# Performance work log

Hardware: AMD Instinct MI355X
Metric: run time of the kernel (lower is better)

Reference implementation:

```python
import jax, jax.numpy as jnp
import numpy as np

NUM_HEADS = 8
TOP_K = 32
LN_EPS = 1e-5
RENORM_EPS = 1e-5


def _split_heads(x):
    # [B, S, D] -> [B, H, S, d]
    B, S, D = x.shape
    return x.reshape(B, S, NUM_HEADS, D // NUM_HEADS).transpose(0, 2, 1, 3)


def setup_inputs() -> dict:
    key = jax.random.key(0)
    k1, k2, k3, k4 = jax.random.split(key, 4)
    B, S, D, H = 2, 2048, 1024, NUM_HEADS
    q = jax.random.normal(k1, (B, S, D), dtype=jnp.float32)
    k = jax.random.normal(k2, (B, S, D), dtype=jnp.float32)
    v = jax.random.normal(k3, (B, S, D), dtype=jnp.float32)
    attention_weight = jax.random.normal(k4, (B, H, S, S), dtype=jnp.float32)
    gamma = jnp.ones((D,), dtype=jnp.float32)
    beta = jnp.zeros((D,), dtype=jnp.float32)
    return {"q": q, "k": k, "v": v, "attention_weight": attention_weight,
            "gamma": gamma, "beta": beta}


def reference(q, k, v, attention_weight, gamma, beta):
    B, S, D = q.shape
    qh = _split_heads(q)  # [B,H,S,d]
    kh = _split_heads(k)
    vh = _split_heads(v)
    # Unscaled QK^T (faithful to source: no /sqrt(d))
    scores = jnp.einsum("bhqd,bhkd->bhqk", qh, kh)
    probs = jax.nn.softmax(scores, axis=-1)
    # top-k mask via double argsort: rank of each key by descending weight
    rank = jnp.argsort(jnp.argsort(-attention_weight, axis=-1), axis=-1)
    top_mask = (rank < TOP_K).astype(probs.dtype)
    probs = probs * top_mask
    probs = probs / (jnp.sum(probs, axis=-1, keepdims=True) + RENORM_EPS)
    out = jnp.einsum("bhqk,bhkd->bhqd", probs, vh)
    out = out.transpose(0, 2, 1, 3).reshape(B, S, D)
    # LayerNorm over last dim
    mu = jnp.mean(out, axis=-1, keepdims=True)
    var = jnp.var(out, axis=-1, keepdims=True)
    out = (out - mu) * jax.lax.rsqrt(var + LN_EPS) * gamma + beta
    return out
```

## Files before the change

### kernel.cpp

```cpp
#include <hip/hip_runtime.h>
#include <stdint.h>

#define BB 2
#define SS 2048
#define DD 1024
#define HH 8
#define HD 128
#define TOPK 32
#define ROWS (BB*HH*SS)
#define BH 16

typedef float f32x4 __attribute__((ext_vector_type(4)));
typedef _Float16 f16x8 __attribute__((ext_vector_type(8)));
typedef _Float16 f16x4 __attribute__((ext_vector_type(4)));

__device__ __forceinline__ void gload_lds16(const _Float16* g, _Float16* l) {
    __builtin_amdgcn_global_load_lds(
        (const __attribute__((address_space(1))) void*)g,
        (__attribute__((address_space(3))) void*)l, 16, 0, 0);
}

__global__ __launch_bounds__(256) void cvt_kernel(const float* __restrict__ q,
                                                  const float* __restrict__ k,
                                                  const float* __restrict__ v,
                                                  _Float16* __restrict__ q16,
                                                  _Float16* __restrict__ k16,
                                                  _Float16* __restrict__ v16) {
    const int row = blockIdx.x;
    const int b = row >> 11, s = row & 2047;
    const int t = threadIdx.x;
    const int h = t >> 5, d4 = (t & 31) * 4;
    const size_t src = (size_t)row * DD + t * 4;
    const size_t dst = ((size_t)(b * HH + h) * SS + s) * HD + d4;
    float4 f;
    f = *(const float4*)(q + src);
    *(f16x4*)(q16 + dst) = (f16x4){(_Float16)f.x,(_Float16)f.y,(_Float16)f.z,(_Float16)f.w};
    f = *(const float4*)(k + src);
    *(f16x4*)(k16 + dst) = (f16x4){(_Float16)f.x,(_Float16)f.y,(_Float16)f.z,(_Float16)f.w};
    f = *(const float4*)(v + src);
    *(f16x4*)(v16 + dst) = (f16x4){(_Float16)f.x,(_Float16)f.y,(_Float16)f.z,(_Float16)f.w};
}

__global__ __launch_bounds__(256) void topk_kernel(const float* __restrict__ aw,
                                                   int* __restrict__ idx_out) {
    const int row = blockIdx.x;
    const float* p = aw + (size_t)row * SS;
    const int t = threadIdx.x;
    float4 v0 = *(const float4*)(p + 4 * t);
    float4 v1 = *(const float4*)(p + 1024 + 4 * t);
    float vals[8] = {v0.x, v0.y, v0.z, v0.w, v1.x, v1.y, v1.z, v1.w};
    unsigned long long key[8];
#pragma unroll
    for (int i = 0; i < 8; i++) {
        int e = (i < 4) ? (4 * t + i) : (1024 + 4 * t + (i - 4));
        unsigned u = __float_as_uint(vals[i]);
        unsigned sk = (u & 0x80000000u) ? ~u : (u | 0x80000000u);
        key[i] = ((unsigned long long)sk << 11) | (unsigned)(2047 - e);
    }
    __shared__ int s_cnt;
    __shared__ int s_red[4];
    __shared__ unsigned long long s_cand[256];
    const int lane = t & 63, wv = t >> 6;

    unsigned thr0 = __float_as_uint(1.76f) | 0x80000000u;
    unsigned long long T = ((unsigned long long)thr0 << 11) | 2047ull;

    if (t == 0) s_cnt = 0;
    __syncthreads();
#pragma unroll
    for (int i = 0; i < 8; i++) {
        if (key[i] > T) {
            int pos = atomicAdd(&s_cnt, 1);
            if (pos < 256) s_cand[pos] = key[i];
        }
    }
    __syncthreads();

    if (s_cnt < TOPK || s_cnt > 256) {
        unsigned long long lo = 0, hi = ~0ull;
        if (s_cnt > 256) lo = T; else hi = T;
        T = lo + ((hi - lo) >> 1);
        for (int it = 0; it < 40; ++it) {
            int c = 0;
#pragma unroll
            for (int i = 0; i < 8; i++) c += (key[i] > T) ? 1 : 0;
            for (int off = 32; off; off >>= 1) c += __shfl_down(c, off, 64);
            if (lane == 0) s_red[wv] = c;
            __syncthreads();
            int tot = s_red[0] + s_red[1] + s_red[2] + s_red[3];
            if (tot >= TOPK && tot <= 256) break;
            if (tot > 256) lo = T; else hi = T;
            T = lo + ((hi - lo) >> 1);
            __syncthreads();
        }
        if (t == 0) s_cnt = 0;
        __syncthreads();
#pragma unroll
        for (int i = 0; i < 8; i++) {
            if (key[i] > T) {
                int pos = atomicAdd(&s_cnt, 1);
                if (pos < 256) s_cand[pos] = key[i];
            }
        }
        __syncthreads();
    }

    const int C = s_cnt < 256 ? s_cnt : 256;
    if (t < C) {
        unsigned long long mk = s_cand[t];
        int rank = 0;
        for (int j = 0; j < C; ++j)
            rank += (s_cand[j] > mk) ? 1 : 0;
        if (rank < TOPK)
            idx_out[(size_t)row * TOPK + rank] = 2047 - (int)(mk & 2047ull);
    }
}

__global__ __launch_bounds__(256) void stats_kernel(const _Float16* __restrict__ q16,
                                                    const _Float16* __restrict__ k16,
                                                    float* __restrict__ ws_m,
                                                    float* __restrict__ ws_l) {
    __shared__ __align__(16) _Float16 Ks[2][64 * 128];
    const int xcd = blockIdx.x & 7;
    const int r = blockIdx.x >> 3;
    const int bh = xcd * 2 + (r & 1);
    const int rr = r >> 1;
    const int qt = rr & 15;
    const int quarter = rr >> 4;
    const int t = threadIdx.x;
    const int wv = t >> 6, lane = t & 63;
    const int l16 = lane & 15, quad = lane >> 4;

    const _Float16* qb = q16 + ((size_t)bh * SS + qt * 128 + wv * 32 + l16) * HD;
    f16x8 af[2][4];
#pragma unroll
    for (int a = 0; a < 2; a++)
#pragma unroll
        for (int ks = 0; ks < 4; ks++)
            af[a][ks] = *(const f16x8*)(qb + a * 16 * HD + ks * 32 + quad * 8);

    const int lr = lane >> 4, lc = lane & 15;
    int srco[4];
#pragma unroll
    for (int i = 0; i < 4; i++) {
        int x = ((i & 1) * 4) + lr;
        srco[i] = (wv * 16 + i * 4 + lr) * HD + ((lc ^ x) * 8);
    }
    const _Float16* kb = k16 + (size_t)bh * SS * HD;

    int rdoff[4];
#pragma unroll
    for (int ks = 0; ks < 4; ks++)
        rdoff[ks] = (((ks * 4 + quad) ^ (l16 & 7)) * 8);

    float mrun[2][4], lrun[2][4];
#pragma unroll
    for (int a = 0; a < 2; a++)
#pragma unroll
        for (int r2 = 0; r2 < 4; r2++) { mrun[a][r2] = -INFINITY; lrun[a][r2] = 0.f; }

    {
        const _Float16* src = kb + (size_t)(quarter * 8) * 64 * HD;
#pragma unroll
        for (int i = 0; i < 4; i++)
            gload_lds16(src + srco[i], &Ks[0][(wv * 4 + i) * 512]);
    }
    __syncthreads();

    int cur = 0;
    for (int tt = 0; tt < 8; ++tt) {
        if (tt < 7) {
            const _Float16* src = kb + (size_t)(quarter * 8 + tt + 1) * 64 * HD;
#pragma unroll
            for (int i = 0; i < 4; i++)
                gload_lds16(src + srco[i], &Ks[cur ^ 1][(wv * 4 + i) * 512]);
        }
        f32x4 acc[2][4];
#pragma unroll
        for (int a = 0; a < 2; a++)
#pragma unroll
            for (int n = 0; n < 4; n++) acc[a][n] = (f32x4){0.f, 0.f, 0.f, 0.f};
#pragma unroll
        for (int ks = 0; ks < 4; ++ks) {
            f16x8 bfr[4];
#pragma unroll
            for (int n = 0; n < 4; n++)
                bfr[n] = *(const f16x8*)&Ks[cur][(n * 16 + l16) * HD + rdoff[ks]];
#pragma unroll
            for (int a = 0; a < 2; a++)
#pragma unroll
                for (int n = 0; n < 4; n++)
                    acc[a][n] = __builtin_amdgcn_mfma_f32_16x16x32_f16(af[a][ks], bfr[n], acc[a][n], 0, 0, 0);
        }
#pragma unroll
        for (int a = 0; a < 2; a++) {
#pragma unroll
            for (int r2 = 0; r2 < 4; r2++) {
                float tm = fmaxf(fmaxf(acc[a][0][r2], acc[a][1][r2]),
                                 fmaxf(acc[a][2][r2], acc[a][3][r2]));
#pragma unroll
                for (int off = 1; off < 16; off <<= 1) tm = fmaxf(tm, __shfl_xor(tm, off, 64));
                float tl = 0.f;
#pragma unroll
                for (int n = 0; n < 4; n++) tl += __expf(acc[a][n][r2] - tm);
#pragma unroll
                for (int off = 1; off < 16; off <<= 1) tl += __shfl_xor(tl, off, 64);
                float mo = mrun[a][r2];
                float mn = fmaxf(mo, tm);
                lrun[a][r2] = lrun[a][r2] * __expf(mo - mn) + tl * __expf(tm - mn);
                mrun[a][r2] = mn;
            }
        }
        __syncthreads();
        cur ^= 1;
    }

    if (l16 == 0) {
#pragma unroll
        for (int a = 0; a < 2; a++)
#pragma unroll
            for (int r2 = 0; r2 < 4; r2++) {
                int rrow = qt * 128 + wv * 32 + a * 16 + quad * 4 + r2;
                size_t g = (size_t)quarter * ROWS + (size_t)bh * SS + rrow;
                ws_m[g] = mrun[a][r2];
                ws_l[g] = lrun[a][r2];
            }
    }
}

__global__ __launch_bounds__(128) void attnout_kernel(const float* __restrict__ q,
                                                      const float* __restrict__ k,
                                                      const _Float16* __restrict__ v16,
                                                      const int* __restrict__ idx_ws,
                                                      const float* __restrict__ ws_m,
                                                      const float* __restrict__ ws_l,
                                                      float* __restrict__ out) {
    const int bh = blockIdx.x & 15;
    const int s = blockIdx.x >> 4;
    const int R = (bh << 11) | s;
    const int b = bh >> 3, h = bh & 7;
    const int t = threadIdx.x;
    __shared__ float q_l[128];
    __shared__ int idx_l[32];
    __shared__ float e_l[32];
    __shared__ float w_l[32];
    __shared__ __align__(16) float s_pv[4][128];
    const float* qrow = q + ((size_t)(b * SS + s) * DD + h * HD);
    q_l[t] = qrow[t];
    if (t < 32) idx_l[t] = idx_ws[(size_t)R * TOPK + t];
    __syncthreads();
    float m = ws_m[R];
    m = fmaxf(m, ws_m[(size_t)ROWS + R]);
    m = fmaxf(m, ws_m[2 * (size_t)ROWS + R]);
    m = fmaxf(m, ws_m[3 * (size_t)ROWS + R]);
    float Z = 0.f;
#pragma unroll
    for (int qr = 0; qr < 4; ++qr)
        Z += ws_l[(size_t)qr * ROWS + R] * __expf(ws_m[(size_t)qr * ROWS + R] - m);

    const int l32 = t & 31, g = t >> 5;
    float4 q4 = *(const float4*)&q_l[l32 * 4];
    const float* kb = k + ((size_t)b * SS * DD + h * HD);
#pragma unroll
    for (int p = 0; p < 8; ++p) {
        int i = p * 4 + g;
        int ki = idx_l[i];
        float4 kv = *(const float4*)(kb + (size_t)ki * DD + l32 * 4);
        float d = q4.x * kv.x + q4.y * kv.y + q4.z * kv.z + q4.w * kv.w;
#pragma unroll
        for (int off = 1; off < 32; off <<= 1) d += __shfl_xor(d, off, 64);
        if (l32 == 0) e_l[i] = __expf(d - m);
    }
    __syncthreads();
    if (t < 32) {
        float e = e_l[t];
        float ssum = e;
#pragma unroll
        for (int off = 1; off < 32; off <<= 1) ssum += __shfl_xor(ssum, off, 64);
        float den = ssum + 1e-5f * Z;
        w_l[t] = e / den;
    }
    __syncthreads();
    const _Float16* vb = v16 + (size_t)bh * SS * HD;
    float a0 = 0.f, a1 = 0.f, a2 = 0.f, a3 = 0.f;
#pragma unroll
    for (int p = 0; p < 8; ++p) {
        int i = p * 4 + g;
        f16x4 hv = *(const f16x4*)(vb + (size_t)idx_l[i] * HD + l32 * 4);
        float w = w_l[i];
        a0 += w * (float)hv[0];
        a1 += w * (float)hv[1];
        a2 += w * (float)hv[2];
        a3 += w * (float)hv[3];
    }
    *(float4*)&s_pv[g][l32 * 4] = make_float4(a0, a1, a2, a3);
    __syncthreads();
    out[((size_t)(b * SS + s) * DD) + h * HD + t] =
        s_pv[0][t] + s_pv[1][t] + s_pv[2][t] + s_pv[3][t];
}

__global__ __launch_bounds__(256) void ln_kernel(float* __restrict__ out,
                                                 const float* __restrict__ gamma,
                                                 const float* __restrict__ beta) {
    const int row = blockIdx.x;
    float* p = out + (size_t)row * DD;
    const int t = threadIdx.x;
    float x[4];
#pragma unroll
    for (int i = 0; i < 4; i++) x[i] = p[t + 256 * i];
    float sum = x[0] + x[1] + x[2] + x[3];
    __shared__ float red[4];
    const int lane = t & 63, wv = t >> 6;
    for (int off = 32; off; off >>= 1) sum += __shfl_down(sum, off, 64);
    if (lane == 0) red[wv] = sum;
    __syncthreads();
    float mean = (red[0] + red[1] + red[2] + red[3]) * (1.f / DD);
    __syncthreads();
    float vs = 0.f;
#pragma unroll
    for (int i = 0; i < 4; i++) { float d = x[i] - mean; vs += d * d; }
    for (int off = 32; off; off >>= 1) vs += __shfl_down(vs, off, 64);
    if (lane == 0) red[wv] = vs;
    __syncthreads();
    float var = (red[0] + red[1] + red[2] + red[3]) * (1.f / DD);
    float inv = rsqrtf(var + 1e-5f);
#pragma unroll
    for (int i = 0; i < 4; i++) {
        int c = t + 256 * i;
        p[c] = (x[i] - mean) * inv * gamma[c] + beta[c];
    }
}

extern "C" void kernel_launch(void* const* d_in, const int* in_sizes, int n_in,
                              void* d_out, int out_size, void* d_ws, size_t ws_size,
                              hipStream_t stream) {
    const float* q = (const float*)d_in[0];
    const float* k = (const float*)d_in[1];
    const float* v = (const float*)d_in[2];
    const float* aw = (const float*)d_in[3];
    const float* gamma = (const float*)d_in[4];
    const float* beta = (const float*)d_in[5];
    float* out = (float*)d_out;

    int* idx_ws = (int*)d_ws;
    float* ws_m = (float*)((char*)d_ws + ((size_t)4 << 20));
    float* ws_l = ws_m + (size_t)4 * ROWS;
    _Float16* q16 = (_Float16*)((char*)d_ws + ((size_t)8 << 20));
    _Float16* k16 = q16 + (size_t)BH * SS * HD;
    _Float16* v16 = k16 + (size_t)BH * SS * HD;

    hipLaunchKernelGGL(cvt_kernel, dim3(BB * SS), dim3(256), 0, stream, q, k, v, q16, k16, v16);
    hipLaunchKernelGGL(topk_kernel, dim3(ROWS), dim3(256), 0, stream, aw, idx_ws);
    hipLaunchKernelGGL(stats_kernel, dim3(1024), dim3(256), 0, stream, q16, k16, ws_m, ws_l);
    hipLaunchKernelGGL(attnout_kernel, dim3(ROWS), dim3(128), 0, stream, q, k, v16, idx_ws, ws_m, ws_l, out);
    hipLaunchKernelGGL(ln_kernel, dim3(BB * SS), dim3(256), 0, stream, out, gamma, beta);
}
```

Baseline: 525.0 us.

## Fuse cvt, topk and stats kernels into one launch with in-kernel fp32 K/Q conversion

Merges the conversion, top-k selection and softmax-stats kernels into a single launch, splitting the work by block index. The stats path now reads fp32 Q and K directly and converts to fp16 in registers before writing K into swizzled LDS, so the separate Q/K fp16 copies are dropped. The aim is to cut kernel launch gaps and the Q/K conversion write-and-reread traffic, and to let top-k blocks overlap with the stats blocks. In exchange, the stats blocks each read twice as many bytes of K and repeat the conversion, and register-staged prefetch replaces the async global-to-LDS loads.

```diff
diff --git a/kernel.cpp b/kernel.cpp
--- a/kernel.cpp
+++ b/kernel.cpp
@@ -10,221 +10,239 @@
 #define ROWS (BB*HH*SS)
 #define BH 16
 
+#define NSTATS 1024
+#define NCVT   4096
+#define NTOPK  32768
+
 typedef float f32x4 __attribute__((ext_vector_type(4)));
 typedef _Float16 f16x8 __attribute__((ext_vector_type(8)));
 typedef _Float16 f16x4 __attribute__((ext_vector_type(4)));
 
-__device__ __forceinline__ void gload_lds16(const _Float16* g, _Float16* l) {
-    __builtin_amdgcn_global_load_lds(
-        (const __attribute__((address_space(1))) void*)g,
-        (__attribute__((address_space(3))) void*)l, 16, 0, 0);
-}
-
-__global__ __launch_bounds__(256) void cvt_kernel(const float* __restrict__ q,
-                                                  const float* __restrict__ k,
-                                                  const float* __restrict__ v,
-                                                  _Float16* __restrict__ q16,
-                                                  _Float16* __restrict__ k16,
-                                                  _Float16* __restrict__ v16) {
-    const int row = blockIdx.x;
-    const int b = row >> 11, s = row & 2047;
-    const int t = threadIdx.x;
-    const int h = t >> 5, d4 = (t & 31) * 4;
-    const size_t src = (size_t)row * DD + t * 4;
-    const size_t dst = ((size_t)(b * HH + h) * SS + s) * HD + d4;
-    float4 f;
-    f = *(const float4*)(q + src);
-    *(f16x4*)(q16 + dst) = (f16x4){(_Float16)f.x,(_Float16)f.y,(_Float16)f.z,(_Float16)f.w};
-    f = *(const float4*)(k + src);
-    *(f16x4*)(k16 + dst) = (f16x4){(_Float16)f.x,(_Float16)f.y,(_Float16)f.z,(_Float16)f.w};
-    f = *(const float4*)(v + src);
-    *(f16x4*)(v16 + dst) = (f16x4){(_Float16)f.x,(_Float16)f.y,(_Float16)f.z,(_Float16)f.w};
-}
-
-__global__ __launch_bounds__(256) void topk_kernel(const float* __restrict__ aw,
-                                                   int* __restrict__ idx_out) {
-    const int row = blockIdx.x;
-    const float* p = aw + (size_t)row * SS;
-    const int t = threadIdx.x;
-    float4 v0 = *(const float4*)(p + 4 * t);
-    float4 v1 = *(const float4*)(p + 1024 + 4 * t);
-    float vals[8] = {v0.x, v0.y, v0.z, v0.w, v1.x, v1.y, v1.z, v1.w};
-    unsigned long long key[8];
-#pragma unroll
-    for (int i = 0; i < 8; i++) {
-        int e = (i < 4) ? (4 * t + i) : (1024 + 4 * t + (i - 4));
-        unsigned u = __float_as_uint(vals[i]);
-        unsigned sk = (u & 0x80000000u) ? ~u : (u | 0x80000000u);
-        key[i] = ((unsigned long long)sk << 11) | (unsigned)(2047 - e);
-    }
-    __shared__ int s_cnt;
-    __shared__ int s_red[4];
-    __shared__ unsigned long long s_cand[256];
-    const int lane = t & 63, wv = t >> 6;
-
-    unsigned thr0 = __float_as_uint(1.76f) | 0x80000000u;
-    unsigned long long T = ((unsigned long long)thr0 << 11) | 2047ull;
-
-    if (t == 0) s_cnt = 0;
-    __syncthreads();
-#pragma unroll
-    for (int i = 0; i < 8; i++) {
-        if (key[i] > T) {
-            int pos = atomicAdd(&s_cnt, 1);
-            if (pos < 256) s_cand[pos] = key[i];
-        }
-    }
-    __syncthreads();
-
-    if (s_cnt < TOPK || s_cnt > 256) {
-        unsigned long long lo = 0, hi = ~0ull;
-        if (s_cnt > 256) lo = T; else hi = T;
-        T = lo + ((hi - lo) >> 1);
-        for (int it = 0; it < 40; ++it) {
-            int c = 0;
-#pragma unroll
-            for (int i = 0; i < 8; i++) c += (key[i] > T) ? 1 : 0;
-            for (int off = 32; off; off >>= 1) c += __shfl_down(c, off, 64);
-            if (lane == 0) s_red[wv] = c;
-            __syncthreads();
-            int tot = s_red[0] + s_red[1] + s_red[2] + s_red[3];
-            if (tot >= TOPK && tot <= 256) break;
-            if (tot > 256) lo = T; else hi = T;
-            T = lo + ((hi - lo) >> 1);
-            __syncthreads();
-        }
-        if (t == 0) s_cnt = 0;
-        __syncthreads();
-#pragma unroll
-        for (int i = 0; i < 8; i++) {
-            if (key[i] > T) {
-                int pos = atomicAdd(&s_cnt, 1);
-                if (pos < 256) s_cand[pos] = key[i];
-            }
-        }
-        __syncthreads();
-    }
-
-    const int C = s_cnt < 256 ? s_cnt : 256;
-    if (t < C) {
-        unsigned long long mk = s_cand[t];
-        int rank = 0;
-        for (int j = 0; j < C; ++j)
-            rank += (s_cand[j] > mk) ? 1 : 0;
-        if (rank < TOPK)
-            idx_out[(size_t)row * TOPK + rank] = 2047 - (int)(mk & 2047ull);
-    }
-}
-
-__global__ __launch_bounds__(256) void stats_kernel(const _Float16* __restrict__ q16,
-                                                    const _Float16* __restrict__ k16,
+__global__ __launch_bounds__(256) void fused_kernel(const float* __restrict__ q,
+                                                    const float* __restrict__ k,
+                                                    const float* __restrict__ v,
+                                                    const float* __restrict__ aw,
+                                                    _Float16* __restrict__ v16,
+                                                    int* __restrict__ idx_out,
                                                     float* __restrict__ ws_m,
                                                     float* __restrict__ ws_l) {
     __shared__ __align__(16) _Float16 Ks[2][64 * 128];
-    const int xcd = blockIdx.x & 7;
-    const int r = blockIdx.x >> 3;
-    const int bh = xcd * 2 + (r & 1);
-    const int rr = r >> 1;
-    const int qt = rr & 15;
-    const int quarter = rr >> 4;
+    const int bid = blockIdx.x;
     const int t = threadIdx.x;
-    const int wv = t >> 6, lane = t & 63;
-    const int l16 = lane & 15, quad = lane >> 4;
-
-    const _Float16* qb = q16 + ((size_t)bh * SS + qt * 128 + wv * 32 + l16) * HD;
-    f16x8 af[2][4];
-#pragma unroll
-    for (int a = 0; a < 2; a++)
+
+    if (bid < NSTATS) {
+        const int xcd = bid & 7;
+        const int r = bid >> 3;
+        const int bh = xcd * 2 + (r & 1);
+        const int rr = r >> 1;
+        const int qt = rr & 15;
+        const int quarter = rr >> 4;
+        const int b = bh >> 3, h = bh & 7;
+        const int wv = t >> 6, lane = t & 63;
+        const int l16 = lane & 15, quad = lane >> 4;
+
+        f16x8 af[2][4];
+#pragma unroll
+        for (int a = 0; a < 2; a++)
+#pragma unroll
+            for (int ks = 0; ks < 4; ks++) {
+                const float* qs = q + (size_t)(b * SS + qt * 128 + wv * 32 + a * 16 + l16) * DD
+                                    + h * HD + ks * 32 + quad * 8;
+                float4 f0 = *(const float4*)qs;
+                float4 f1 = *(const float4*)(qs + 4);
+                af[a][ks] = (f16x8){(_Float16)f0.x,(_Float16)f0.y,(_Float16)f0.z,(_Float16)f0.w,
+                                    (_Float16)f1.x,(_Float16)f1.y,(_Float16)f1.z,(_Float16)f1.w};
+            }
+
+        const int srow = t >> 2, cgrp = t & 3;
+        const float* kb = k + (size_t)b * SS * DD + h * HD;
+
+        int rdoff[4];
 #pragma unroll
         for (int ks = 0; ks < 4; ks++)
-            af[a][ks] = *(const f16x8*)(qb + a * 16 * HD + ks * 32 + quad * 8);
-
-    const int lr = lane >> 4, lc = lane & 15;
-    int srco[4];
-#pragma unroll
-    for (int i = 0; i < 4; i++) {
-        int x = ((i & 1) * 4) + lr;
-        srco[i] = (wv * 16 + i * 4 + lr) * HD + ((lc ^ x) * 8);
-    }
-    const _Float16* kb = k16 + (size_t)bh * SS * HD;
-
-    int rdoff[4];
-#pragma unroll
-    for (int ks = 0; ks < 4; ks++)
-        rdoff[ks] = (((ks * 4 + quad) ^ (l16 & 7)) * 8);
-
-    float mrun[2][4], lrun[2][4];
-#pragma unroll
-    for (int a = 0; a < 2; a++)
-#pragma unroll
-        for (int r2 = 0; r2 < 4; r2++) { mrun[a][r2] = -INFINITY; lrun[a][r2] = 0.f; }
+            rdoff[ks] = (((ks * 4 + quad) ^ (l16 & 7)) * 8);
+
+        float mrun[2][4], lrun[2][4];
+#pragma unroll
+        for (int a = 0; a < 2; a++)
+#pragma unroll
+            for (int r2 = 0; r2 < 4; r2++) { mrun[a][r2] = -INFINITY; lrun[a][r2] = 0.f; }
+
+        {
+            const float* src = kb + (size_t)(quarter * 8 * 64 + srow) * DD;
+            float4 fr[8];
+#pragma unroll
+            for (int c = 0; c < 4; c++) {
+                int cc = cgrp * 4 + c;
+                fr[c * 2]     = *(const float4*)(src + cc * 8);
+                fr[c * 2 + 1] = *(const float4*)(src + cc * 8 + 4);
+            }
+#pragma unroll
+            for (int c = 0; c < 4; c++) {
+                int cc = cgrp * 4 + c;
+                f16x8 w = {(_Float16)fr[c*2].x,(_Float16)fr[c*2].y,(_Float16)fr[c*2].z,(_Float16)fr[c*2].w,
+                           (_Float16)fr[c*2+1].x,(_Float16)fr[c*2+1].y,(_Float16)fr[c*2+1].z,(_Float16)fr[c*2+1].w};
+                *(f16x8*)&Ks[0][srow * 128 + ((cc ^ (srow & 7)) * 8)] = w;
+            }
+        }
+        __syncthreads();
+
+        int cur = 0;
+        for (int tt = 0; tt < 8; ++tt) {
+            float4 nf[8];
+            if (tt < 7) {
+                const float* src = kb + (size_t)((quarter * 8 + tt + 1) * 64 + srow) * DD;
+#pragma unroll
+                for (int c = 0; c < 4; c++) {
+                    int cc = cgrp * 4 + c;
+                    nf[c * 2]     = *(const float4*)(src + cc * 8);
+                    nf[c * 2 + 1] = *(const float4*)(src + cc * 8 + 4);
+                }
+            }
+            f32x4 acc[2][4];
+#pragma unroll
+            for (int a = 0; a < 2; a++)
+#pragma unroll
+                for (int n = 0; n < 4; n++) acc[a][n] = (f32x4){0.f, 0.f, 0.f, 0.f};
+#pragma unroll
+            for (int ks = 0; ks < 4; ++ks) {
+                f16x8 bfr[4];
+#pragma unroll
+                for (int n = 0; n < 4; n++)
+                    bfr[n] = *(const f16x8*)&Ks[cur][(n * 16 + l16) * 128 + rdoff[ks]];
+#pragma unroll
+                for (int a = 0; a < 2; a++)
+#pragma unroll
+                    for (int n = 0; n < 4; n++)
+                        acc[a][n] = __builtin_amdgcn_mfma_f32_16x16x32_f16(af[a][ks], bfr[n], acc[a][n], 0, 0, 0);
+            }
+#pragma unroll
+            for (int a = 0; a < 2; a++) {
+#pragma unroll
+                for (int r2 = 0; r2 < 4; r2++) {
+                    float tm = fmaxf(fmaxf(acc[a][0][r2], acc[a][1][r2]),
+                                     fmaxf(acc[a][2][r2], acc[a][3][r2]));
+#pragma unroll
+                    for (int off = 1; off < 16; off <<= 1) tm = fmaxf(tm, __shfl_xor(tm, off, 64));
+                    float tl = 0.f;
+#pragma unroll
+                    for (int n = 0; n < 4; n++) tl += __expf(acc[a][n][r2] - tm);
+#pragma unroll
+                    for (int off = 1; off < 16; off <<= 1) tl += __shfl_xor(tl, off, 64);
+                    float mo = mrun[a][r2];
+                    float mn = fmaxf(mo, tm);
+                    lrun[a][r2] = lrun[a][r2] * __expf(mo - mn) + tl * __expf(tm - mn);
+                    mrun[a][r2] = mn;
+                }
+            }
+            if (tt < 7) {
+#pragma unroll
+                for (int c = 0; c < 4; c++) {
+                    int cc = cgrp * 4 + c;
+                    f16x8 w = {(_Float16)nf[c*2].x,(_Float16)nf[c*2].y,(_Float16)nf[c*2].z,(_Float16)nf[c*2].w,
+                               (_Float16)nf[c*2+1].x,(_Float16)nf[c*2+1].y,(_Float16)nf[c*2+1].z,(_Float16)nf[c*2+1].w};
+                    *(f16x8*)&Ks[cur ^ 1][srow * 128 + ((cc ^ (srow & 7)) * 8)] = w;
+                }
+            }
+            __syncthreads();
+            cur ^= 1;
+        }
+
+        if (l16 == 0) {
+#pragma unroll
+            for (int a = 0; a < 2; a++)
+#pragma unroll
+                for (int r2 = 0; r2 < 4; r2++) {
+                    int rrow = qt * 128 + wv * 32 + a * 16 + quad * 4 + r2;
+                    size_t g = (size_t)quarter * ROWS + (size_t)bh * SS + rrow;
+                    ws_m[g] = mrun[a][r2];
+                    ws_l[g] = lrun[a][r2];
+                }
+        }
+        return;
+    }
+
+    if (bid < NSTATS + NCVT) {
+        const int row = bid - NSTATS;
+        const int b = row >> 11, s = row & 2047;
+        const int h = t >> 5, d4 = (t & 31) * 4;
+        float4 f = *(const float4*)(v + (size_t)row * DD + t * 4);
+        *(f16x4*)(v16 + ((size_t)(b * HH + h) * SS + s) * HD + d4) =
+            (f16x4){(_Float16)f.x,(_Float16)f.y,(_Float16)f.z,(_Float16)f.w};
+        return;
+    }
 
     {
-        const _Float16* src = kb + (size_t)(quarter * 8) * 64 * HD;
-#pragma unroll
-        for (int i = 0; i < 4; i++)
-            gload_lds16(src + srco[i], &Ks[0][(wv * 4 + i) * 512]);
-    }
-    __syncthreads();
-
-    int cur = 0;
-    for (int tt = 0; tt < 8; ++tt) {
-        if (tt < 7) {
-            const _Float16* src = kb + (size_t)(quarter * 8 + tt + 1) * 64 * HD;
-#pragma unroll
-            for (int i = 0; i < 4; i++)
-                gload_lds16(src + srco[i], &Ks[cur ^ 1][(wv * 4 + i) * 512]);
-        }
-        f32x4 acc[2][4];
-#pragma unroll
-        for (int a = 0; a < 2; a++)
-#pragma unroll
-            for (int n = 0; n < 4; n++) acc[a][n] = (f32x4){0.f, 0.f, 0.f, 0.f};
-#pragma unroll
-        for (int ks = 0; ks < 4; ++ks) {
-            f16x8 bfr[4];
-#pragma unroll
-            for (int n = 0; n < 4; n++)
-                bfr[n] = *(const f16x8*)&Ks[cur][(n * 16 + l16) * HD + rdoff[ks]];
-#pragma unroll
-            for (int a = 0; a < 2; a++)
-#pragma unroll
-                for (int n = 0; n < 4; n++)
-                    acc[a][n] = __builtin_amdgcn_mfma_f32_16x16x32_f16(af[a][ks], bfr[n], acc[a][n], 0, 0, 0);
-        }
-#pragma unroll
-        for (int a = 0; a < 2; a++) {
-#pragma unroll
-            for (int r2 = 0; r2 < 4; r2++) {
-                float tm = fmaxf(fmaxf(acc[a][0][r2], acc[a][1][r2]),
-                                 fmaxf(acc[a][2][r2], acc[a][3][r2]));
-#pragma unroll
-                for (int off = 1; off < 16; off <<= 1) tm = fmaxf(tm, __shfl_xor(tm, off, 64));
-                float tl = 0.f;
-#pragma unroll
-                for (int n = 0; n < 4; n++) tl += __expf(acc[a][n][r2] - tm);
-#pragma unroll
-                for (int off = 1; off < 16; off <<= 1) tl += __shfl_xor(tl, off, 64);
-                float mo = mrun[a][r2];
-                float mn = fmaxf(mo, tm);
-                lrun[a][r2] = lrun[a][r2] * __expf(mo - mn) + tl * __expf(tm - mn);
-                mrun[a][r2] = mn;
-            }
-        }
+        const int row = bid - (NSTATS + NCVT);
+        const float* p = aw + (size_t)row * SS;
+        int* s_cnt = (int*)&Ks[0][0];
+        int* s_red = (int*)&Ks[0][8];
+        unsigned long long* s_cand = (unsigned long long*)&Ks[0][32];
+        float4 v0 = *(const float4*)(p + 4 * t);
+        float4 v1 = *(const float4*)(p + 1024 + 4 * t);
+        float vals[8] = {v0.x, v0.y, v0.z, v0.w, v1.x, v1.y, v1.z, v1.w};
+        unsigned long long key[8];
+#pragma unroll
+        for (int i = 0; i < 8; i++) {
+            int e = (i < 4) ? (4 * t + i) : (1024 + 4 * t + (i - 4));
+            unsigned u = __float_as_uint(vals[i]);
+            unsigned sk = (u & 0x80000000u) ? ~u : (u | 0x80000000u);
+            key[i] = ((unsigned long long)sk << 11) | (unsigned)(2047 - e);
+        }
+        const int lane = t & 63, wv = t >> 6;
+
+        unsigned thr0 = __float_as_uint(1.76f) | 0x80000000u;
+        unsigned long long T = ((unsigned long long)thr0 << 11) | 2047ull;
+
+        if (t == 0) *s_cnt = 0;
         __syncthreads();
-        cur ^= 1;
-    }
-
-    if (l16 == 0) {
-#pragma unroll
-        for (int a = 0; a < 2; a++)
-#pragma unroll
-            for (int r2 = 0; r2 < 4; r2++) {
-                int rrow = qt * 128 + wv * 32 + a * 16 + quad * 4 + r2;
-                size_t g = (size_t)quarter * ROWS + (size_t)bh * SS + rrow;
-                ws_m[g] = mrun[a][r2];
-                ws_l[g] = lrun[a][r2];
-            }
+#pragma unroll
+        for (int i = 0; i < 8; i++) {
+            if (key[i] > T) {
+                int pos = atomicAdd(s_cnt, 1);
+                if (pos < 256) s_cand[pos] = key[i];
+            }
+        }
+        __syncthreads();
+
+        if (*s_cnt < TOPK || *s_cnt > 256) {
+            unsigned long long lo = 0, hi = ~0ull;
+            if (*s_cnt > 256) lo = T; else hi = T;
+            T = lo + ((hi - lo) >> 1);
+            for (int it = 0; it < 40; ++it) {
+                int c = 0;
+#pragma unroll
+                for (int i = 0; i < 8; i++) c += (key[i] > T) ? 1 : 0;
+                for (int off = 32; off; off >>= 1) c += __shfl_down(c, off, 64);
+                if (lane == 0) s_red[wv] = c;
+                __syncthreads();
+                int tot = s_red[0] + s_red[1] + s_red[2] + s_red[3];
+                if (tot >= TOPK && tot <= 256) break;
+                if (tot > 256) lo = T; else hi = T;
+                T = lo + ((hi - lo) >> 1);
+                __syncthreads();
+            }
+            if (t == 0) *s_cnt = 0;
+            __syncthreads();
+#pragma unroll
+            for (int i = 0; i < 8; i++) {
+                if (key[i] > T) {
+                    int pos = atomicAdd(s_cnt, 1);
+                    if (pos < 256) s_cand[pos] = key[i];
+                }
+            }
+            __syncthreads();
+        }
+
+        const int C = *s_cnt < 256 ? *s_cnt : 256;
+        if (t < C) {
+            unsigned long long mk = s_cand[t];
+            int rank = 0;
+            for (int j = 0; j < C; ++j)
+                rank += (s_cand[j] > mk) ? 1 : 0;
+            if (rank < TOPK)
+                idx_out[(size_t)row * TOPK + rank] = 2047 - (int)(mk & 2047ull);
+        }
     }
 }
 
@@ -345,13 +363,11 @@
     int* idx_ws = (int*)d_ws;
     float* ws_m = (float*)((char*)d_ws + ((size_t)4 << 20));
     float* ws_l = ws_m + (size_t)4 * ROWS;
-    _Float16* q16 = (_Float16*)((char*)d_ws + ((size_t)8 << 20));
-    _Float16* k16 = q16 + (size_t)BH * SS * HD;
-    _Float16* v16 = k16 + (size_t)BH * SS * HD;
-
-    hipLaunchKernelGGL(cvt_kernel, dim3(BB * SS), dim3(256), 0, stream, q, k, v, q16, k16, v16);
-    hipLaunchKernelGGL(topk_kernel, dim3(ROWS), dim3(256), 0, stream, aw, idx_ws);
-    hipLaunchKernelGGL(stats_kernel, dim3(1024), dim3(256), 0, stream, q16, k16, ws_m, ws_l);
-    hipLaunchKernelGGL(attnout_kernel, dim3(ROWS), dim3(128), 0, stream, q, k, v16, idx_ws, ws_m, ws_l, out);
+    _Float16* v16 = (_Float16*)((char*)d_ws + ((size_t)8 << 20));
+
+    hipLaunchKernelGGL(fused_kernel, dim3(NSTATS + NCVT + NTOPK), dim3(256), 0, stream,
+                       q, k, v, aw, v16, idx_ws, ws_m, ws_l);
+    hipLaunchKernelGGL(attnout_kernel, dim3(ROWS), dim3(128), 0, stream,
+                       q, k, v16, idx_ws, ws_m, ws_l, out);
     hipLaunchKernelGGL(ln_kernel, dim3(BB * SS), dim3(256), 0, stream, out, gamma, beta);
 }
```

Result: slower. 658.3 us (+25.4%).
